# Optimization experiments

Hardware: AMD Instinct MI355X
Metric: run time of the kernel (lower is better)

Reference implementation:

```python
import jax, jax.numpy as jnp
import numpy as np
from jax import lax

B, C, H, W = 8, 256, 64, 64
NUM_HEADS = 4
HEAD_DIM = C // NUM_HEADS  # == dim // 4, required by q_proj
EPS_LN = 1e-5
EPS_NORM = 1e-12


def _gelu(x):
    return jax.nn.gelu(x, approximate=False)  # torch default GELU is erf-based


def setup_inputs() -> dict:
    key = jax.random.key(0)
    ks = jax.random.split(key, 20)
    s = lambda fan_in: 1.0 / np.sqrt(fan_in)
    return {
        "x": jax.random.normal(ks[0], (B, C, H, W), jnp.float32),
        # LayerNorm(dim)
        "ln_g": jnp.ones((C,), jnp.float32),
        "ln_b": jnp.zeros((C,), jnp.float32),
        # qkv: Linear(C, 3C, bias=False); stored (in, out)
        "w_qkv": jax.random.normal(ks[1], (C, 3 * C), jnp.float32) * s(C),
        # q_proj: Linear(head_dim, head_dim); stored (in, out)
        "w_q": jax.random.normal(ks[2], (HEAD_DIM, HEAD_DIM), jnp.float32) * s(HEAD_DIM),
        "b_q": jax.random.normal(ks[3], (HEAD_DIM,), jnp.float32) * 0.01,
        "temperature": jnp.ones((NUM_HEADS, 1, 1), jnp.float32),
        # depthwise 3x3 conv, groups=C: kernel (C,1,3,3) OIHW
        "dw_w": jax.random.normal(ks[4], (C, 1, 3, 3), jnp.float32) * s(9),
        "dw_b": jax.random.normal(ks[5], (C,), jnp.float32) * 0.01,
        # channel_interaction: 1x1 convs stored as (out, in)
        "ci_w1": jax.random.normal(ks[6], (C // 8, C), jnp.float32) * s(C),
        "ci_b1": jax.random.normal(ks[7], (C // 8,), jnp.float32) * 0.01,
        "ci_w2": jax.random.normal(ks[8], (C, C // 8), jnp.float32) * s(C // 8),
        "ci_b2": jax.random.normal(ks[9], (C,), jnp.float32) * 0.01,
        # spatial_interaction: 1x1 convs stored as (out, in)
        "si_w1": jax.random.normal(ks[10], (C // 16, C), jnp.float32) * s(C),
        "si_b1": jax.random.normal(ks[11], (C // 16,), jnp.float32) * 0.01,
        "si_w2": jax.random.normal(ks[12], (1, C // 16), jnp.float32) * s(C // 16),
        "si_b2": jax.random.normal(ks[13], (1,), jnp.float32) * 0.01,
        # proj: Linear(C, C); stored (in, out)
        "proj_w": jax.random.normal(ks[14], (C, C), jnp.float32) * s(C),
        "proj_b": jax.random.normal(ks[15], (C,), jnp.float32) * 0.01,
    }


def reference(x, ln_g, ln_b, w_qkv, w_q, b_q, temperature, dw_w, dw_b,
              ci_w1, ci_b1, ci_w2, ci_b2, si_w1, si_b1, si_w2, si_b2,
              proj_w, proj_b):
    Bx, Cx, Hx, Wx = x.shape
    N = Hx * Wx
    nh = temperature.shape[0]
    hd = Cx // nh

    # before_RG: (B,C,H,W) -> (B,N,C), LayerNorm over C
    xt = x.reshape(Bx, Cx, N).transpose(0, 2, 1)
    mu = xt.mean(-1, keepdims=True)
    var = ((xt - mu) ** 2).mean(-1, keepdims=True)
    xn = (xt - mu) * lax.rsqrt(var + EPS_LN) * ln_g + ln_b

    # qkv -> (3, B, nh, N, hd)
    qkv = (xn @ w_qkv).reshape(Bx, N, 3, nh, hd).transpose(2, 0, 3, 1, 4)
    q, k, v = qkv[0], qkv[1], qkv[2]
    q = q @ w_q + b_q                      # Linear on head_dim
    q = q.transpose(0, 1, 3, 2)            # (B, nh, hd, N)
    k = k.transpose(0, 1, 3, 2)
    v = v.transpose(0, 1, 3, 2)
    v_ = v.reshape(Bx, Cx, Hx, Wx)         # head-major channel layout

    # L2 normalize along N (torch F.normalize semantics)
    q = q / jnp.clip(jnp.linalg.norm(q, axis=-1, keepdims=True), EPS_NORM)
    k = k / jnp.clip(jnp.linalg.norm(k, axis=-1, keepdims=True), EPS_NORM)

    # channel attention: (B, nh, hd, hd)
    attn = jnp.einsum('bhdn,bhen->bhde', q, k) * temperature
    attn = jax.nn.softmax(attn, axis=-1)
    attened_x = jnp.einsum('bhde,bhen->bhdn', attn, v)
    attened_x = attened_x.transpose(0, 3, 1, 2).reshape(Bx, N, Cx)  # (B,N,C)

    # depthwise conv branch + GELU
    conv_x = lax.conv_general_dilated(
        v_, dw_w, window_strides=(1, 1), padding='SAME',
        feature_group_count=Cx, dimension_numbers=('NCHW', 'OIHW', 'NCHW'))
    conv_x = _gelu(conv_x + dw_b[None, :, None, None])

    # channel interaction (SE on attention branch)
    pooled = attened_x.mean(axis=1)                    # (B,C) == global avg pool of (B,C,H,W)
    ci = _gelu(pooled @ ci_w1.T + ci_b1)
    channel_map = ci @ ci_w2.T + ci_b2                 # (B,C)

    # spatial interaction (on conv branch)
    si = _gelu(jnp.einsum('bchw,oc->bohw', conv_x, si_w1) + si_b1[None, :, None, None])
    spatial_map = jnp.einsum('bchw,oc->bohw', si, si_w2) + si_b2[None, :, None, None]  # (B,1,H,W)
    spatial_map = spatial_map.reshape(Bx, N, 1)

    # cross gating and fuse
    attened_x = attened_x * jax.nn.sigmoid(spatial_map)
    conv_x = conv_x * jax.nn.sigmoid(channel_map)[:, :, None, None]
    conv_x = conv_x.reshape(Bx, Cx, N).transpose(0, 2, 1)

    out = (attened_x + conv_x) @ proj_w + proj_b       # (B,N,C)
    return out.transpose(0, 2, 1).reshape(Bx, Cx, Hx, Wx)
```

## Files before the change

### kernel.cpp

```cpp
#include <hip/hip_runtime.h>

typedef unsigned short u16;
typedef short bf16x8 __attribute__((ext_vector_type(8)));
typedef float f32x4 __attribute__((ext_vector_type(4)));

__device__ __forceinline__ float bf2f(u16 u){ return __uint_as_float(((unsigned)u)<<16); }
__device__ __forceinline__ u16 f2bf(float f){
  unsigned u = __float_as_uint(f);
  u += 0x7FFF + ((u >> 16) & 1);
  return (u16)(u >> 16);
}
__device__ __forceinline__ float ldp(const void* p, size_t i, int bf){
  return bf ? bf2f(((const u16*)p)[i]) : ((const float*)p)[i];
}
__device__ __forceinline__ float gelu_f(float x){ return 0.5f*x*(1.0f+erff(x*0.70710678118654752440f)); }
__device__ __forceinline__ float sigmoid_f(float x){ return 1.0f/(1.0f+expf(-x)); }

struct __align__(8)  U16x4 { u16 x,y,z,w; };
struct __align__(16) U16x8 { u16 v[8]; };

#define Cc 256
#define Nn 4096
#define CN 1048576


__global__ void k_flag(const unsigned* __restrict__ g_bits, int* __restrict__ flag){
  if (threadIdx.x == 0)
    *flag = (g_bits[0] == 0x3F803F80u) ? 1 : 0;
}

__global__ void k_zero(float* __restrict__ p){
  size_t i = ((size_t)blockIdx.x*256 + threadIdx.x)*4;
  float4 z; z.x=0.f; z.y=0.f; z.z=0.f; z.w=0.f;
  *(float4*)(p + i) = z;
}

__global__ void k_prep(const void* __restrict__ wqkv, const void* __restrict__ wq,
                       const void* __restrict__ bq, const void* __restrict__ pw,
                       const int* __restrict__ flag,
                       u16* __restrict__ WallT16, u16* __restrict__ pwT16,
                       float* __restrict__ biasall){
  int bf = *flag;
  int j = blockIdx.x;
  int c = threadIdx.x;
  if (j < 768){
    float out;
    if (j < 256){
      int h = j >> 6, e = j & 63;
      float acc = 0.f;
      #pragma unroll 8
      for (int d = 0; d < 64; ++d)
        acc += ldp(wqkv, c*768 + h*64 + d, bf) * ldp(wq, d*64 + e, bf);
      out = acc;
    } else {
      out = ldp(wqkv, c*768 + j, bf);
    }
    size_t a = ((size_t)((j>>4)*8 + (c>>5))*64 + (j&15) + 16*((c>>3)&3))*8 + (c&7);
    WallT16[a] = f2bf(out);
    if (c == 0) biasall[j] = (j < 256) ? ldp(bq, j & 63, bf) : 0.f;
  } else {
    int o = j - 768;
    size_t a = ((size_t)((o>>4)*8 + (c>>5))*64 + (o&15) + 16*((c>>3)&3))*8 + (c&7);
    pwT16[a] = f2bf(ldp(pw, c*256 + o, bf));
  }
}

__global__ __launch_bounds__(256) void k_lnT(const void* __restrict__ x,
                    const void* __restrict__ g, const void* __restrict__ bta,
                    const int* __restrict__ flag,
                    u16* __restrict__ xn16){
  __shared__ float tile[256*65];
  __shared__ float gs[256], bs[256];
  __shared__ float red_s[4][64], red_ss[4][64];
  __shared__ float mu_sh[64], rs_sh[64];
  int bf = *flag;
  int tid = threadIdx.x;
  int b  = blockIdx.x >> 6;
  int n0 = (blockIdx.x & 63) * 64;
  gs[tid] = ldp(g, tid, bf); bs[tid] = ldp(bta, tid, bf);
  int crow = tid >> 2, noff = (tid & 3) * 16;
  for (int p = 0; p < 4; ++p){
    int c = p*64 + crow;
    size_t base = (size_t)b*CN + (size_t)c*Nn + n0 + noff;
    float vals[16];
    if (bf){
      #pragma unroll
      for (int q = 0; q < 2; ++q){
        U16x8 u = *(const U16x8*)((const u16*)x + base + q*8);
        #pragma unroll
        for (int i = 0; i < 8; ++i) vals[q*8+i] = bf2f(u.v[i]);
      }
    } else {
      #pragma unroll
      for (int q = 0; q < 4; ++q){
        float4 f = *(const float4*)((const float*)x + base + q*4);
        vals[q*4+0]=f.x; vals[q*4+1]=f.y; vals[q*4+2]=f.z; vals[q*4+3]=f.w;
      }
    }
    #pragma unroll
    for (int i = 0; i < 16; ++i) tile[c*65 + noff + i] = vals[i];
  }
  __syncthreads();
  {
    int r = tid >> 6, nl = tid & 63;
    float s = 0.f, ss = 0.f;
    for (int cc = r*64; cc < r*64 + 64; ++cc){
      float v = tile[cc*65 + nl];
      s += v; ss += v*v;
    }
    red_s[r][nl] = s; red_ss[r][nl] = ss;
  }
  __syncthreads();
  if (tid < 64){
    float st  = red_s[0][tid]  + red_s[1][tid]  + red_s[2][tid]  + red_s[3][tid];
    float sst = red_ss[0][tid] + red_ss[1][tid] + red_ss[2][tid] + red_ss[3][tid];
    float m   = st * (1.f/256.f);
    float var = sst * (1.f/256.f) - m*m;
    mu_sh[tid] = m;
    rs_sh[tid] = rsqrtf(var + 1e-5f);
  }
  __syncthreads();
  int n = tid >> 2, coff = (tid & 3) * 64;
  float mn = mu_sh[n], rn = rs_sh[n];
  int gidx = (n0 >> 4) + (n >> 4);
  int l15 = n & 15;
  u16* dstb = xn16 + ((size_t)b*256 + gidx)*4096;
  for (int q = 0; q < 8; ++q){
    int c8 = coff + q*8;
    int ks = c8 >> 5, quad = (c8 >> 3) & 3;
    U16x8 w;
    #pragma unroll
    for (int i = 0; i < 8; ++i){
      int c = c8 + i;
      w.v[i] = f2bf((tile[c*65 + n] - mn)*rn*gs[c] + bs[c]);
    }
    *(U16x8*)(dstb + (size_t)ks*512 + (l15 + 16*quad)*8) = w;
  }
}

__global__ __launch_bounds__(256, 4) void k_qkv(const u16* __restrict__ xn16,
                                             const u16* __restrict__ WallT16,
                                             const float* __restrict__ biasall,
                                             u16* __restrict__ q16, u16* __restrict__ k16,
                                             u16* __restrict__ v16, u16* __restrict__ vT16,
                                             float* __restrict__ qsq, float* __restrict__ ksq){
  __shared__ u16 Bs[16384];
  __shared__ float bias_sh[64];
  __shared__ float sq_sh[64];
  int tid = threadIdx.x;
  int by = blockIdx.x;
  int bx = blockIdx.y;
  int b  = by >> 5;
  int n0 = (by & 31) * 128;
  int j0 = bx * 64;
  int part = bx >> 2;
  int h = (j0 >> 6) & 3;
  int w = tid >> 6, lane = tid & 63, l15 = lane & 15, quad = lane >> 4;

  const u16* Afrag = xn16 + ((size_t)b*256 + (n0>>4) + w*2)*4096 + lane*8;
  bf16x8 af[2][8];
  #pragma unroll
  for (int r = 0; r < 2; ++r)
    #pragma unroll
    for (int ks = 0; ks < 8; ++ks)
      af[r][ks] = *(const bf16x8*)(Afrag + (size_t)r*4096 + (size_t)ks*512);

  const u16* Bt = WallT16 + (size_t)(j0>>4)*4096;
  #pragma unroll
  for (int i = 0; i < 8; ++i){
    int off = (i*256 + tid)*8;
    *(bf16x8*)(Bs + off) = *(const bf16x8*)(Bt + off);
  }
  if (tid < 64){ bias_sh[tid] = biasall[j0 + tid]; sq_sh[tid] = 0.f; }
  __syncthreads();

  f32x4 acc[2][4];
  #pragma unroll
  for (int r=0;r<2;++r)
    #pragma unroll
    for (int s=0;s<4;++s){ acc[r][s][0]=0.f; acc[r][s][1]=0.f; acc[r][s][2]=0.f; acc[r][s][3]=0.f; }

  const u16* Bfrag = Bs + lane*8;
  #pragma unroll
  for (int ks = 0; ks < 8; ++ks){
    #pragma unroll
    for (int s = 0; s < 4; ++s){
      bf16x8 bb = *(const bf16x8*)(Bfrag + s*4096 + ks*512);
      acc[0][s] = __builtin_amdgcn_mfma_f32_16x16x32_bf16(af[0][ks], bb, acc[0][s], 0, 0, 0);
      acc[1][s] = __builtin_amdgcn_mfma_f32_16x16x32_bf16(af[1][ks], bb, acc[1][s], 0, 0, 0);
    }
  }
  u16* dst = (part==0) ? q16 : ((part==1) ? k16 : v16);
  float sql[4];
  #pragma unroll
  for (int s=0;s<4;++s) sql[s]=0.f;
  #pragma unroll
  for (int r = 0; r < 2; ++r){
    int nb = n0 + w*32 + r*16 + quad*4;
    #pragma unroll
    for (int s = 0; s < 4; ++s){
      int d = s*16 + l15;
      float bd = bias_sh[d];
      float v0 = acc[r][s][0] + bd, v1 = acc[r][s][1] + bd;
      float v2 = acc[r][s][2] + bd, v3 = acc[r][s][3] + bd;
      U16x4 wv; wv.x=f2bf(v0); wv.y=f2bf(v1); wv.z=f2bf(v2); wv.w=f2bf(v3);
      *(U16x4*)(dst + ((size_t)(b*4 + h)*64 + d)*4096 + nb) = wv;
      sql[s] += v0*v0 + v1*v1 + v2*v2 + v3*v3;
    }
  }
  if (part < 2){
    #pragma unroll
    for (int s = 0; s < 4; ++s)
      atomicAdd(&sq_sh[s*16 + l15], sql[s]);
    __syncthreads();
    if (tid < 64){
      float* nsq = (part==0) ? qsq : ksq;
      atomicAdd(&nsq[(b*4 + h)*64 + tid], sq_sh[tid]);
    }
  } else {
    __syncthreads();
    u16* Ls = Bs;
    #pragma unroll
    for (int r = 0; r < 2; ++r){
      #pragma unroll
      for (int s = 0; s < 4; ++s){
        int d = s*16 + l15;
        #pragma unroll
        for (int i = 0; i < 4; ++i){
          int nl = w*32 + r*16 + quad*4 + i;
          Ls[nl*72 + d] = f2bf(acc[r][s][i]);
        }
      }
    }
    __syncthreads();
    u16* vt = vT16 + ((size_t)(b*4 + h))*262144 + (size_t)(n0>>4)*1024;
    #pragma unroll
    for (int it = 0; it < 4; ++it){
      int lin = it*256 + tid;
      int t15 = lin & 15, q4 = (lin>>4)&3, ks = (lin>>6)&1, g = lin>>7;
      int nl = g*16 + t15;
      int e0 = ks*32 + q4*8;
      U16x8 wv = *(const U16x8*)&Ls[nl*72 + e0];
      *(U16x8*)(vt + (size_t)lin*8) = wv;
    }
  }
}

__global__ __launch_bounds__(256) void k_attnp(const u16* __restrict__ q16,
                                               const u16* __restrict__ k16,
                                               float* __restrict__ S){
  int tid = threadIdx.x;
  int bh = blockIdx.y;
  int kc = blockIdx.x;
  int w = tid >> 6, lane = tid & 63, l15 = lane & 15, quad = lane >> 4;
  f32x4 acc[4];
  #pragma unroll
  for (int s=0;s<4;++s){ acc[s][0]=0.f; acc[s][1]=0.f; acc[s][2]=0.f; acc[s][3]=0.f; }
  const u16* qp = q16 + ((size_t)bh*64 + w*16 + l15)*4096 + quad*8;
  const u16* kp = k16 + ((size_t)bh*64 + l15)*4096 + quad*8;
  #pragma unroll 4
  for (int nn = kc*512; nn < kc*512 + 512; nn += 32){
    bf16x8 a = *(const bf16x8*)(qp + nn);
    #pragma unroll
    for (int s = 0; s < 4; ++s){
      bf16x8 bb = *(const bf16x8*)(kp + (size_t)s*16*4096 + nn);
      acc[s] = __builtin_amdgcn_mfma_f32_16x16x32_bf16(a, bb, acc[s], 0, 0, 0);
    }
  }
  float* Sb = S + (size_t)bh*4096;
  #pragma unroll
  for (int s = 0; s < 4; ++s)
    #pragma unroll
    for (int i = 0; i < 4; ++i)
      atomicAdd(&Sb[(w*16 + quad*4 + i)*64 + s*16 + l15], acc[s][i]);
}

__global__ __launch_bounds__(256) void k_softmax(float* __restrict__ S,
                          const float* __restrict__ qsq, const float* __restrict__ ksq,
                          const void* __restrict__ temp, const int* __restrict__ flag,
                          u16* __restrict__ P16){
  __shared__ float kn_sh[64], qn_sh[64];
  int bf = *flag;
  int bh = blockIdx.x;
  int tid = threadIdx.x;
  if (tid < 64){
    kn_sh[tid] = fmaxf(sqrtf(ksq[bh*64 + tid]), 1e-12f);
    qn_sh[tid] = fmaxf(sqrtf(qsq[bh*64 + tid]), 1e-12f);
  }
  __syncthreads();
  int d  = tid >> 2;
  int e0 = (tid & 3) * 16;
  float tpr = ldp(temp, bh & 3, bf);
  const float* row = S + (size_t)bh*4096 + d*64 + e0;
  float sc = tpr / qn_sh[d];
  float v[16];
  #pragma unroll
  for (int q = 0; q < 4; ++q){
    float4 f = *(const float4*)(row + q*4);
    v[q*4+0]=f.x; v[q*4+1]=f.y; v[q*4+2]=f.z; v[q*4+3]=f.w;
  }
  float mx = -1e30f;
  #pragma unroll
  for (int e = 0; e < 16; ++e){
    v[e] = v[e] * sc / kn_sh[e0 + e];
    mx = fmaxf(mx, v[e]);
  }
  mx = fmaxf(mx, __shfl_xor(mx, 1));
  mx = fmaxf(mx, __shfl_xor(mx, 2));
  float s = 0.f;
  #pragma unroll
  for (int e = 0; e < 16; ++e){ v[e] = expf(v[e] - mx); s += v[e]; }
  s += __shfl_xor(s, 1);
  s += __shfl_xor(s, 2);
  float inv = 1.f/s;
  u16* pb16 = P16 + bh*4096;
  int g = d >> 4, l15d = d & 15;
  #pragma unroll
  for (int half = 0; half < 2; ++half){
    int e = e0 + half*8;
    int ks = e >> 5, q4 = (e >> 3) & 3;
    U16x8 wv;
    #pragma unroll
    for (int i = 0; i < 8; ++i) wv.v[i] = f2bf(v[half*8 + i]*inv);
    *(U16x8*)(pb16 + ((g*2 + ks)*64 + l15d + 16*q4)*8) = wv;
  }
}

__global__ __launch_bounds__(256) void k_av(const u16* __restrict__ P16,
                                            const u16* __restrict__ vT16,
                                            u16* __restrict__ attT,
                                            float* __restrict__ pooled){
  __shared__ u16 Bs[16384];
  __shared__ float red[64];
  int bh = blockIdx.y;
  int n0 = blockIdx.x * 256;
  int tid = threadIdx.x, w = tid >> 6, lane = tid & 63, l15 = lane & 15, quad = lane >> 4;
  int b = bh >> 2, h = bh & 3;
  const u16* vt = vT16 + (size_t)bh*262144 + (size_t)(n0>>4)*1024;
  #pragma unroll
  for (int i = 0; i < 8; ++i){
    int off = (i*256 + tid)*8;
    *(bf16x8*)(Bs + off) = *(const bf16x8*)(vt + off);
  }
  if (tid < 64) red[tid] = 0.f;
  const u16* pp = P16 + bh*4096;
  bf16x8 af0 = *(const bf16x8*)(pp + ((w*2 + 0)*64 + lane)*8);
  bf16x8 af1 = *(const bf16x8*)(pp + ((w*2 + 1)*64 + lane)*8);
  __syncthreads();
  f32x4 acc[16];
  #pragma unroll
  for (int s = 0; s < 16; ++s){ acc[s][0]=0.f; acc[s][1]=0.f; acc[s][2]=0.f; acc[s][3]=0.f; }
  const u16* Bfrag = Bs + lane*8;
  #pragma unroll
  for (int s = 0; s < 16; ++s){
    bf16x8 b0 = *(const bf16x8*)(Bfrag + (s*2 + 0)*512);
    bf16x8 b1 = *(const bf16x8*)(Bfrag + (s*2 + 1)*512);
    acc[s] = __builtin_amdgcn_mfma_f32_16x16x32_bf16(af0, b0, acc[s], 0, 0, 0);
    acc[s] = __builtin_amdgcn_mfma_f32_16x16x32_bf16(af1, b1, acc[s], 0, 0, 0);
  }
  u16* ob = attT + ((size_t)b*4096 + n0)*256 + h*64 + w*16 + quad*4;
  float p0=0.f, p1=0.f, p2=0.f, p3=0.f;
  #pragma unroll
  for (int s = 0; s < 16; ++s){
    int n = s*16 + l15;
    U16x4 wv; wv.x=f2bf(acc[s][0]); wv.y=f2bf(acc[s][1]); wv.z=f2bf(acc[s][2]); wv.w=f2bf(acc[s][3]);
    *(U16x4*)(ob + (size_t)n*256) = wv;
    p0 += acc[s][0]; p1 += acc[s][1]; p2 += acc[s][2]; p3 += acc[s][3];
  }
  atomicAdd(&red[w*16 + quad*4 + 0], p0);
  atomicAdd(&red[w*16 + quad*4 + 1], p1);
  atomicAdd(&red[w*16 + quad*4 + 2], p2);
  atomicAdd(&red[w*16 + quad*4 + 3], p3);
  __syncthreads();
  if (tid < 64)
    atomicAdd(&pooled[b*256 + h*64 + tid], red[tid]);
}

__global__ void k_conv(const u16* __restrict__ v16, const void* __restrict__ dww,
                       const void* __restrict__ dwb, const int* __restrict__ flag,
                       u16* __restrict__ conv16){
  __shared__ float plane[4096];
  int bf = *flag;
  int bc = blockIdx.x;
  int c = bc & 255;
  int tid = threadIdx.x;
  const u16* vp = v16 + (size_t)bc*4096;
  #pragma unroll
  for (int i = 0; i < 4; ++i){
    int lin = (i*256 + tid)*4;
    U16x4 vu = *(const U16x4*)(vp + lin);
    plane[lin+0]=bf2f(vu.x); plane[lin+1]=bf2f(vu.y); plane[lin+2]=bf2f(vu.z); plane[lin+3]=bf2f(vu.w);
  }
  float wgt[9];
  #pragma unroll
  for (int i = 0; i < 9; ++i) wgt[i] = ldp(dww, c*9 + i, bf);
  float bias = ldp(dwb, c, bf);
  __syncthreads();
  u16* op = conv16 + (size_t)bc*4096;
  for (int it = 0; it < 16; ++it){
    int p = it*256 + tid;
    int y = p >> 6, x = p & 63;
    float acc = bias;
    #pragma unroll
    for (int ky = 0; ky < 3; ++ky){
      int yy = y + ky - 1;
      if (yy < 0 || yy > 63) continue;
      #pragma unroll
      for (int kx = 0; kx < 3; ++kx){
        int xx = x + kx - 1;
        if (xx < 0 || xx > 63) continue;
        acc += wgt[ky*3+kx]*plane[yy*64 + xx];
      }
    }
    op[p] = f2bf(gelu_f(acc));
  }
}

__global__ __launch_bounds__(256) void k_spatial(const u16* __restrict__ conv16,
                                                 const void* __restrict__ w1, const void* __restrict__ b1,
                                                 const void* __restrict__ w2, const void* __restrict__ b2,
                                                 const int* __restrict__ flag,
                                                 float* __restrict__ ssp){
  __shared__ float w1s[16][256];
  __shared__ u16 tile[256][72];
  __shared__ float red[4][64][17];
  int bf = *flag;
  int tid = threadIdx.x;
  for (int i = 0; i < 16; ++i)
    w1s[i][tid] = ldp(w1, i*256 + tid, bf);
  int b  = blockIdx.x >> 6;
  int n0 = (blockIdx.x & 63) * 64;
  const u16* cb = conv16 + (size_t)b*CN + n0;
  #pragma unroll
  for (int i = 0; i < 8; ++i){
    int idx = i*256 + tid;
    int c = idx >> 3, seg = idx & 7;
    *(U16x8*)&tile[c][seg*8] = *(const U16x8*)(cb + (size_t)c*Nn + seg*8);
  }
  __syncthreads();
  int nl = tid & 63, r = tid >> 6;
  float acc[16] = {};
  for (int cc = r*64; cc < r*64 + 64; ++cc){
    float xv = bf2f(tile[cc][nl]);
    #pragma unroll
    for (int o = 0; o < 16; ++o) acc[o] += xv * w1s[o][cc];
  }
  #pragma unroll
  for (int o = 0; o < 16; ++o) red[r][nl][o] = acc[o];
  __syncthreads();
  if (tid < 64){
    float sp = ldp(b2, 0, bf);
    #pragma unroll
    for (int o = 0; o < 16; ++o){
      float a = red[0][tid][o] + red[1][tid][o] + red[2][tid][o] + red[3][tid][o];
      sp += gelu_f(a + ldp(b1, o, bf)) * ldp(w2, o, bf);
    }
    ssp[(size_t)b*Nn + n0 + tid] = sigmoid_f(sp);
  }
}

__global__ void k_channel(const float* __restrict__ pooled,
                          const void* __restrict__ w1, const void* __restrict__ b1,
                          const void* __restrict__ w2, const void* __restrict__ b2,
                          const int* __restrict__ flag,
                          float* __restrict__ sch){
  __shared__ float ps[256];
  __shared__ float cis[32];
  int bf = *flag;
  int b = blockIdx.x, tid = threadIdx.x;
  ps[tid] = pooled[b*256 + tid] * (1.f/4096.f);
  __syncthreads();
  if (tid < 32){
    float a = ldp(b1, tid, bf);
    for (int cc = 0; cc < 256; ++cc) a += ps[cc]*ldp(w1, tid*256 + cc, bf);
    cis[tid] = gelu_f(a);
  }
  __syncthreads();
  float m = ldp(b2, tid, bf);
  #pragma unroll
  for (int o = 0; o < 32; ++o) m += cis[o]*ldp(w2, tid*32 + o, bf);
  sch[b*256 + tid] = sigmoid_f(m);
}

__global__ __launch_bounds__(256) void k_gate(const u16* __restrict__ attT,
                                              const u16* __restrict__ conv16,
                                              const float* __restrict__ ssp,
                                              const float* __restrict__ sch,
                                              u16* __restrict__ Y16){
  __shared__ u16 ct[256*66];
  __shared__ u16 at[64*264];
  __shared__ float ssp_sh[64], sch_sh[256];
  int tid = threadIdx.x;
  int b  = blockIdx.x >> 6;
  int n0 = (blockIdx.x & 63) * 64;
  sch_sh[tid] = sch[b*256 + tid];
  if (tid < 64) ssp_sh[tid] = ssp[(size_t)b*Nn + n0 + tid];
  const u16* cb = conv16 + (size_t)b*CN + n0;
  #pragma unroll
  for (int i = 0; i < 8; ++i){
    int idx = i*256 + tid;
    int c = idx >> 3, seg = idx & 7;
    *(U16x8*)&ct[c*66 + seg*8] = *(const U16x8*)(cb + (size_t)c*Nn + seg*8);
  }
  const u16* ab = attT + ((size_t)b*4096 + n0)*256;
  #pragma unroll
  for (int i = 0; i < 8; ++i){
    int idx = i*256 + tid;
    int n = idx >> 5, seg = idx & 31;
    *(U16x8*)&at[n*264 + seg*8] = *(const U16x8*)(ab + (size_t)n*256 + seg*8);
  }
  __syncthreads();
  u16* dstb = Y16 + ((size_t)b*256 + (n0>>4))*4096;
  #pragma unroll
  for (int it = 0; it < 8; ++it){
    int lin = it*256 + tid;
    int l15 = lin & 15, q4 = (lin>>4)&3, ks = (lin>>6)&7, ng = lin>>9;
    int n = ng*16 + l15;
    int c0 = ks*32 + q4*8;
    float gn = ssp_sh[n];
    U16x8 av = *(const U16x8*)&at[n*264 + c0];
    U16x8 wv;
    #pragma unroll
    for (int i = 0; i < 8; ++i){
      int c = c0 + i;
      wv.v[i] = f2bf(bf2f(av.v[i])*gn + bf2f(ct[c*66 + n])*sch_sh[c]);
    }
    *(U16x8*)(dstb + (size_t)lin*8) = wv;
  }
}

__global__ __launch_bounds__(256, 4) void k_proj(const u16* __restrict__ Y16,
                                              const u16* __restrict__ pwT16,
                                              const void* __restrict__ pb,
                                              const int* __restrict__ flag,
                                              void* __restrict__ out){
  __shared__ u16 Bs[16384];
  __shared__ float pb_sh[64];
  int bf = *flag;
  int tid = threadIdx.x;
  int by = blockIdx.x;
  int bx = blockIdx.y;
  int b  = by >> 5;
  int n0 = (by & 31) * 128;
  int c0 = bx * 64;
  int w = tid >> 6, lane = tid & 63, l15 = lane & 15, quad = lane >> 4;

  const u16* Afrag = Y16 + ((size_t)b*256 + (n0>>4) + w*2)*4096 + lane*8;
  bf16x8 af[2][8];
  #pragma unroll
  for (int r = 0; r < 2; ++r)
    #pragma unroll
    for (int ks = 0; ks < 8; ++ks)
      af[r][ks] = *(const bf16x8*)(Afrag + (size_t)r*4096 + (size_t)ks*512);

  const u16* Bt = pwT16 + (size_t)(c0>>4)*4096;
  #pragma unroll
  for (int i = 0; i < 8; ++i){
    int off = (i*256 + tid)*8;
    *(bf16x8*)(Bs + off) = *(const bf16x8*)(Bt + off);
  }
  if (tid < 64) pb_sh[tid] = ldp(pb, c0 + tid, bf);
  __syncthreads();

  f32x4 acc[2][4];
  #pragma unroll
  for (int r=0;r<2;++r)
    #pragma unroll
    for (int s=0;s<4;++s){ acc[r][s][0]=0.f; acc[r][s][1]=0.f; acc[r][s][2]=0.f; acc[r][s][3]=0.f; }

  const u16* Bfrag = Bs + lane*8;
  #pragma unroll
  for (int ks = 0; ks < 8; ++ks){
    #pragma unroll
    for (int s = 0; s < 4; ++s){
      bf16x8 bb = *(const bf16x8*)(Bfrag + s*4096 + ks*512);
      acc[0][s] = __builtin_amdgcn_mfma_f32_16x16x32_bf16(af[0][ks], bb, acc[0][s], 0, 0, 0);
      acc[1][s] = __builtin_amdgcn_mfma_f32_16x16x32_bf16(af[1][ks], bb, acc[1][s], 0, 0, 0);
    }
  }
  #pragma unroll
  for (int r = 0; r < 2; ++r){
    int nb = n0 + w*32 + r*16 + quad*4;
    #pragma unroll
    for (int s = 0; s < 4; ++s){
      int cch = c0 + s*16 + l15;
      float pbias = pb_sh[s*16 + l15];
      size_t oidx = ((size_t)(b*256 + cch))*4096 + nb;
      float v0 = acc[r][s][0] + pbias, v1 = acc[r][s][1] + pbias;
      float v2 = acc[r][s][2] + pbias, v3 = acc[r][s][3] + pbias;
      if (bf){
        U16x4 wv; wv.x=f2bf(v0); wv.y=f2bf(v1); wv.z=f2bf(v2); wv.w=f2bf(v3);
        *(U16x4*)((u16*)out + oidx) = wv;
      } else {
        float4 wv; wv.x=v0; wv.y=v1; wv.z=v2; wv.w=v3;
        *(float4*)((float*)out + oidx) = wv;
      }
    }
  }
}

extern "C" void kernel_launch(void* const* d_in, const int* in_sizes, int n_in,
                              void* d_out, int out_size, void* d_ws, size_t ws_size,
                              hipStream_t stream) {
  const void* x    = d_in[0];
  const void* ln_g = d_in[1];
  const void* ln_b = d_in[2];
  const void* wqkv = d_in[3];
  const void* wq   = d_in[4];
  const void* bq   = d_in[5];
  const void* temp = d_in[6];
  const void* dww  = d_in[7];
  const void* dwb  = d_in[8];
  const void* ciw1 = d_in[9];
  const void* cib1 = d_in[10];
  const void* ciw2 = d_in[11];
  const void* cib2 = d_in[12];
  const void* siw1 = d_in[13];
  const void* sib1 = d_in[14];
  const void* siw2 = d_in[15];
  const void* sib2 = d_in[16];
  const void* pw   = d_in[17];
  const void* pb   = d_in[18];

  u16* wsu    = (u16*)d_ws;
  u16* q16    = wsu;
  u16* k16    = wsu + 8388608;
  u16* xn16   = wsu + 16777216;
  u16* attT   = q16;
  u16* conv16 = k16;
  u16* Y16    = xn16;
  u16* v16    = (u16*)d_out;

  u16* vT16;
  if (out_size >= 33554432) vT16 = (u16*)d_out + 8388608;
  else                      vT16 = wsu + 25165824;

  float* tail = (float*)(wsu + 33554432);
  float* qsq  = tail;
  float* ksq  = qsq + 2048;
  float* S    = ksq + 2048;
  float* pool = S + 131072;
  float* biasall = pool + 2048;
  float* sch  = biasall + 768;
  float* ssp  = sch + 2048;
  u16* P16     = (u16*)(ssp + 32768);
  u16* WallT16 = P16 + 131072;
  u16* pwT16   = WallT16 + 196608;
  int* flag    = (int*)(pwT16 + 65536);

  hipLaunchKernelGGL(k_flag,  dim3(1), dim3(64), 0, stream, (const unsigned*)ln_g, flag);
  hipLaunchKernelGGL(k_zero,  dim3(134), dim3(256), 0, stream, qsq);
  hipLaunchKernelGGL(k_prep,  dim3(1024), dim3(256), 0, stream, wqkv, wq, bq, pw, flag, WallT16, pwT16, biasall);
  hipLaunchKernelGGL(k_lnT,   dim3(512), dim3(256), 0, stream, x, ln_g, ln_b, flag, xn16);
  hipLaunchKernelGGL(k_qkv,   dim3(256, 12), dim3(256), 0, stream,
                     xn16, WallT16, biasall, q16, k16, v16, vT16, qsq, ksq);
  hipLaunchKernelGGL(k_attnp, dim3(8, 32), dim3(256), 0, stream, q16, k16, S);
  hipLaunchKernelGGL(k_softmax, dim3(32), dim3(256), 0, stream, S, qsq, ksq, temp, flag, P16);
  hipLaunchKernelGGL(k_av,    dim3(16, 32), dim3(256), 0, stream, P16, vT16, attT, pool);
  hipLaunchKernelGGL(k_conv,  dim3(2048), dim3(256), 0, stream, v16, dww, dwb, flag, conv16);
  hipLaunchKernelGGL(k_spatial, dim3(512), dim3(256), 0, stream, conv16, siw1, sib1, siw2, sib2, flag, ssp);
  hipLaunchKernelGGL(k_channel, dim3(8), dim3(256), 0, stream, pool, ciw1, cib1, ciw2, cib2, flag, sch);
  hipLaunchKernelGGL(k_gate,  dim3(512), dim3(256), 0, stream, attT, conv16, ssp, sch, Y16);
  hipLaunchKernelGGL(k_proj,  dim3(256, 4), dim3(256), 0, stream, Y16, pwT16, pb, flag, d_out);
}
```

Measured before the change: 291.4 us.

## Fuse attention stages, gate+projection, and inline dtype flag; vectorize depthwise conv

Merges the three attention kernels (partial QK^T with global atomics, softmax, AV) into one per-(batch,head) kernel that keeps scores and probabilities in shared memory. It also fuses the gating kernel into the output projection, keeping the gated tile in LDS. The flag and zero kernels are removed: the dtype test is done inline and zeroing moves into the prep kernel. The depthwise conv now computes 16 outputs per thread from register rows. The fused attention kernel runs only 32 blocks, so GPU occupancy drops sharply in exchange for fewer launches and fewer global round trips.

```diff
diff --git a/kernel.cpp b/kernel.cpp
--- a/kernel.cpp
+++ b/kernel.cpp
@@ -15,6 +15,7 @@
 }
 __device__ __forceinline__ float gelu_f(float x){ return 0.5f*x*(1.0f+erff(x*0.70710678118654752440f)); }
 __device__ __forceinline__ float sigmoid_f(float x){ return 1.0f/(1.0f+expf(-x)); }
+__device__ __forceinline__ int bfdet(const void* g){ return ((const unsigned*)g)[0] == 0x3F803F80u; }
 
 struct __align__(8)  U16x4 { u16 x,y,z,w; };
 struct __align__(16) U16x8 { u16 v[8]; };
@@ -24,25 +25,20 @@
 #define CN 1048576
 
 
-__global__ void k_flag(const unsigned* __restrict__ g_bits, int* __restrict__ flag){
-  if (threadIdx.x == 0)
-    *flag = (g_bits[0] == 0x3F803F80u) ? 1 : 0;
-}
-
-__global__ void k_zero(float* __restrict__ p){
-  size_t i = ((size_t)blockIdx.x*256 + threadIdx.x)*4;
-  float4 z; z.x=0.f; z.y=0.f; z.z=0.f; z.w=0.f;
-  *(float4*)(p + i) = z;
-}
-
 __global__ void k_prep(const void* __restrict__ wqkv, const void* __restrict__ wq,
                        const void* __restrict__ bq, const void* __restrict__ pw,
-                       const int* __restrict__ flag,
+                       const unsigned* __restrict__ g_bits,
                        u16* __restrict__ WallT16, u16* __restrict__ pwT16,
-                       float* __restrict__ biasall){
-  int bf = *flag;
+                       float* __restrict__ biasall, float* __restrict__ zbase){
   int j = blockIdx.x;
   int c = threadIdx.x;
+  if (j >= 1024){
+    size_t i = (size_t)(j - 1024)*1024 + c*4;
+    float4 z; z.x=0.f; z.y=0.f; z.z=0.f; z.w=0.f;
+    *(float4*)(zbase + i) = z;
+    return;
+  }
+  int bf = bfdet(g_bits);
   if (j < 768){
     float out;
     if (j < 256){
@@ -67,13 +63,12 @@
 
 __global__ __launch_bounds__(256) void k_lnT(const void* __restrict__ x,
                     const void* __restrict__ g, const void* __restrict__ bta,
-                    const int* __restrict__ flag,
                     u16* __restrict__ xn16){
   __shared__ float tile[256*65];
   __shared__ float gs[256], bs[256];
   __shared__ float red_s[4][64], red_ss[4][64];
   __shared__ float mu_sh[64], rs_sh[64];
-  int bf = *flag;
+  int bf = bfdet(g);
   int tid = threadIdx.x;
   int b  = blockIdx.x >> 6;
   int n0 = (blockIdx.x & 63) * 64;
@@ -246,20 +241,38 @@
   }
 }
 
-__global__ __launch_bounds__(256) void k_attnp(const u16* __restrict__ q16,
-                                               const u16* __restrict__ k16,
-                                               float* __restrict__ S){
+__global__ __launch_bounds__(512) void k_attn(const u16* __restrict__ q16,
+                                              const u16* __restrict__ k16,
+                                              const u16* __restrict__ vT16,
+                                              const float* __restrict__ qsq,
+                                              const float* __restrict__ ksq,
+                                              const void* __restrict__ temp,
+                                              const unsigned* __restrict__ g_bits,
+                                              u16* __restrict__ attT,
+                                              float* __restrict__ pooled){
+  __shared__ float S_sh[2][64][68];
+  __shared__ u16 P_sh[4096];
+  __shared__ float kn_sh[64], qn_sh[64];
+  __shared__ float red[64];
+  int bf = bfdet(g_bits);
+  int bh = blockIdx.x; int b = bh >> 2, h = bh & 3;
   int tid = threadIdx.x;
-  int bh = blockIdx.y;
-  int kc = blockIdx.x;
-  int w = tid >> 6, lane = tid & 63, l15 = lane & 15, quad = lane >> 4;
+  int w2 = tid >> 6, lane = tid & 63, l15 = lane & 15, quad = lane >> 4;
+  int dg = w2 & 3, nh = w2 >> 2;
+
+  if (tid < 64){
+    kn_sh[tid] = fmaxf(sqrtf(ksq[bh*64 + tid]), 1e-12f);
+    qn_sh[tid] = fmaxf(sqrtf(qsq[bh*64 + tid]), 1e-12f);
+    red[tid] = 0.f;
+  }
+
   f32x4 acc[4];
   #pragma unroll
   for (int s=0;s<4;++s){ acc[s][0]=0.f; acc[s][1]=0.f; acc[s][2]=0.f; acc[s][3]=0.f; }
-  const u16* qp = q16 + ((size_t)bh*64 + w*16 + l15)*4096 + quad*8;
-  const u16* kp = k16 + ((size_t)bh*64 + l15)*4096 + quad*8;
+  const u16* qp = q16 + ((size_t)bh*64 + dg*16 + l15)*4096 + quad*8 + nh*2048;
+  const u16* kp = k16 + ((size_t)bh*64 + l15)*4096 + quad*8 + nh*2048;
   #pragma unroll 4
-  for (int nn = kc*512; nn < kc*512 + 512; nn += 32){
+  for (int nn = 0; nn < 2048; nn += 32){
     bf16x8 a = *(const bf16x8*)(qp + nn);
     #pragma unroll
     for (int s = 0; s < 4; ++s){
@@ -267,120 +280,87 @@
       acc[s] = __builtin_amdgcn_mfma_f32_16x16x32_bf16(a, bb, acc[s], 0, 0, 0);
     }
   }
-  float* Sb = S + (size_t)bh*4096;
   #pragma unroll
   for (int s = 0; s < 4; ++s)
     #pragma unroll
     for (int i = 0; i < 4; ++i)
-      atomicAdd(&Sb[(w*16 + quad*4 + i)*64 + s*16 + l15], acc[s][i]);
-}
-
-__global__ __launch_bounds__(256) void k_softmax(float* __restrict__ S,
-                          const float* __restrict__ qsq, const float* __restrict__ ksq,
-                          const void* __restrict__ temp, const int* __restrict__ flag,
-                          u16* __restrict__ P16){
-  __shared__ float kn_sh[64], qn_sh[64];
-  int bf = *flag;
-  int bh = blockIdx.x;
-  int tid = threadIdx.x;
-  if (tid < 64){
-    kn_sh[tid] = fmaxf(sqrtf(ksq[bh*64 + tid]), 1e-12f);
-    qn_sh[tid] = fmaxf(sqrtf(qsq[bh*64 + tid]), 1e-12f);
-  }
-  __syncthreads();
-  int d  = tid >> 2;
-  int e0 = (tid & 3) * 16;
-  float tpr = ldp(temp, bh & 3, bf);
-  const float* row = S + (size_t)bh*4096 + d*64 + e0;
-  float sc = tpr / qn_sh[d];
-  float v[16];
-  #pragma unroll
-  for (int q = 0; q < 4; ++q){
-    float4 f = *(const float4*)(row + q*4);
-    v[q*4+0]=f.x; v[q*4+1]=f.y; v[q*4+2]=f.z; v[q*4+3]=f.w;
-  }
-  float mx = -1e30f;
-  #pragma unroll
-  for (int e = 0; e < 16; ++e){
-    v[e] = v[e] * sc / kn_sh[e0 + e];
-    mx = fmaxf(mx, v[e]);
-  }
-  mx = fmaxf(mx, __shfl_xor(mx, 1));
-  mx = fmaxf(mx, __shfl_xor(mx, 2));
-  float s = 0.f;
-  #pragma unroll
-  for (int e = 0; e < 16; ++e){ v[e] = expf(v[e] - mx); s += v[e]; }
-  s += __shfl_xor(s, 1);
-  s += __shfl_xor(s, 2);
-  float inv = 1.f/s;
-  u16* pb16 = P16 + bh*4096;
-  int g = d >> 4, l15d = d & 15;
-  #pragma unroll
-  for (int half = 0; half < 2; ++half){
-    int e = e0 + half*8;
-    int ks = e >> 5, q4 = (e >> 3) & 3;
+      S_sh[nh][dg*16 + quad*4 + i][s*16 + l15] = acc[s][i];
+  __syncthreads();
+
+  {
+    int d = tid >> 3, el = tid & 7, e0 = el*8;
+    float tpr = ldp(temp, h, bf);
+    float sc = tpr / qn_sh[d];
+    float v[8];
+    float4 a0 = *(const float4*)&S_sh[0][d][e0];
+    float4 a1 = *(const float4*)&S_sh[0][d][e0+4];
+    float4 b0 = *(const float4*)&S_sh[1][d][e0];
+    float4 b1 = *(const float4*)&S_sh[1][d][e0+4];
+    v[0]=a0.x+b0.x; v[1]=a0.y+b0.y; v[2]=a0.z+b0.z; v[3]=a0.w+b0.w;
+    v[4]=a1.x+b1.x; v[5]=a1.y+b1.y; v[6]=a1.z+b1.z; v[7]=a1.w+b1.w;
+    float mx = -1e30f;
+    #pragma unroll
+    for (int e = 0; e < 8; ++e){
+      v[e] = v[e] * sc / kn_sh[e0 + e];
+      mx = fmaxf(mx, v[e]);
+    }
+    mx = fmaxf(mx, __shfl_xor(mx, 1));
+    mx = fmaxf(mx, __shfl_xor(mx, 2));
+    mx = fmaxf(mx, __shfl_xor(mx, 4));
+    float s = 0.f;
+    #pragma unroll
+    for (int e = 0; e < 8; ++e){ v[e] = expf(v[e] - mx); s += v[e]; }
+    s += __shfl_xor(s, 1);
+    s += __shfl_xor(s, 2);
+    s += __shfl_xor(s, 4);
+    float inv = 1.f/s;
+    int g = d >> 4, l15d = d & 15, ks = el >> 2, q4 = el & 3;
     U16x8 wv;
     #pragma unroll
-    for (int i = 0; i < 8; ++i) wv.v[i] = f2bf(v[half*8 + i]*inv);
-    *(U16x8*)(pb16 + ((g*2 + ks)*64 + l15d + 16*q4)*8) = wv;
-  }
-}
-
-__global__ __launch_bounds__(256) void k_av(const u16* __restrict__ P16,
-                                            const u16* __restrict__ vT16,
-                                            u16* __restrict__ attT,
-                                            float* __restrict__ pooled){
-  __shared__ u16 Bs[16384];
-  __shared__ float red[64];
-  int bh = blockIdx.y;
-  int n0 = blockIdx.x * 256;
-  int tid = threadIdx.x, w = tid >> 6, lane = tid & 63, l15 = lane & 15, quad = lane >> 4;
-  int b = bh >> 2, h = bh & 3;
-  const u16* vt = vT16 + (size_t)bh*262144 + (size_t)(n0>>4)*1024;
-  #pragma unroll
-  for (int i = 0; i < 8; ++i){
-    int off = (i*256 + tid)*8;
-    *(bf16x8*)(Bs + off) = *(const bf16x8*)(vt + off);
-  }
-  if (tid < 64) red[tid] = 0.f;
-  const u16* pp = P16 + bh*4096;
-  bf16x8 af0 = *(const bf16x8*)(pp + ((w*2 + 0)*64 + lane)*8);
-  bf16x8 af1 = *(const bf16x8*)(pp + ((w*2 + 1)*64 + lane)*8);
-  __syncthreads();
-  f32x4 acc[16];
-  #pragma unroll
-  for (int s = 0; s < 16; ++s){ acc[s][0]=0.f; acc[s][1]=0.f; acc[s][2]=0.f; acc[s][3]=0.f; }
-  const u16* Bfrag = Bs + lane*8;
-  #pragma unroll
-  for (int s = 0; s < 16; ++s){
-    bf16x8 b0 = *(const bf16x8*)(Bfrag + (s*2 + 0)*512);
-    bf16x8 b1 = *(const bf16x8*)(Bfrag + (s*2 + 1)*512);
-    acc[s] = __builtin_amdgcn_mfma_f32_16x16x32_bf16(af0, b0, acc[s], 0, 0, 0);
-    acc[s] = __builtin_amdgcn_mfma_f32_16x16x32_bf16(af1, b1, acc[s], 0, 0, 0);
-  }
-  u16* ob = attT + ((size_t)b*4096 + n0)*256 + h*64 + w*16 + quad*4;
-  float p0=0.f, p1=0.f, p2=0.f, p3=0.f;
-  #pragma unroll
-  for (int s = 0; s < 16; ++s){
-    int n = s*16 + l15;
-    U16x4 wv; wv.x=f2bf(acc[s][0]); wv.y=f2bf(acc[s][1]); wv.z=f2bf(acc[s][2]); wv.w=f2bf(acc[s][3]);
-    *(U16x4*)(ob + (size_t)n*256) = wv;
-    p0 += acc[s][0]; p1 += acc[s][1]; p2 += acc[s][2]; p3 += acc[s][3];
-  }
-  atomicAdd(&red[w*16 + quad*4 + 0], p0);
-  atomicAdd(&red[w*16 + quad*4 + 1], p1);
-  atomicAdd(&red[w*16 + quad*4 + 2], p2);
-  atomicAdd(&red[w*16 + quad*4 + 3], p3);
+    for (int i = 0; i < 8; ++i) wv.v[i] = f2bf(v[i]*inv);
+    *(U16x8*)(P_sh + ((g*2 + ks)*64 + l15d + 16*q4)*8) = wv;
+  }
+  __syncthreads();
+
+  bf16x8 af[4][2];
+  #pragma unroll
+  for (int mg = 0; mg < 4; ++mg)
+    #pragma unroll
+    for (int ks = 0; ks < 2; ++ks)
+      af[mg][ks] = *(const bf16x8*)(P_sh + ((mg*2 + ks)*64 + lane)*8);
+  const u16* vt = vT16 + (size_t)bh*262144;
+  float ps[4][4] = {};
+  for (int g64 = 0; g64 < 32; ++g64){
+    int gidx = w2*32 + g64;
+    bf16x8 b0 = *(const bf16x8*)(vt + (size_t)gidx*1024 + lane*8);
+    bf16x8 b1 = *(const bf16x8*)(vt + (size_t)gidx*1024 + 512 + lane*8);
+    int n = gidx*16 + l15;
+    u16* ob = attT + ((size_t)b*4096 + n)*256 + h*64 + quad*4;
+    #pragma unroll
+    for (int mg = 0; mg < 4; ++mg){
+      f32x4 o; o[0]=0.f; o[1]=0.f; o[2]=0.f; o[3]=0.f;
+      o = __builtin_amdgcn_mfma_f32_16x16x32_bf16(af[mg][0], b0, o, 0, 0, 0);
+      o = __builtin_amdgcn_mfma_f32_16x16x32_bf16(af[mg][1], b1, o, 0, 0, 0);
+      U16x4 wv; wv.x=f2bf(o[0]); wv.y=f2bf(o[1]); wv.z=f2bf(o[2]); wv.w=f2bf(o[3]);
+      *(U16x4*)(ob + mg*16) = wv;
+      ps[mg][0] += o[0]; ps[mg][1] += o[1]; ps[mg][2] += o[2]; ps[mg][3] += o[3];
+    }
+  }
+  #pragma unroll
+  for (int mg = 0; mg < 4; ++mg)
+    #pragma unroll
+    for (int i = 0; i < 4; ++i)
+      atomicAdd(&red[mg*16 + quad*4 + i], ps[mg][i]);
   __syncthreads();
   if (tid < 64)
     atomicAdd(&pooled[b*256 + h*64 + tid], red[tid]);
 }
 
-__global__ void k_conv(const u16* __restrict__ v16, const void* __restrict__ dww,
-                       const void* __restrict__ dwb, const int* __restrict__ flag,
+__global__ __launch_bounds__(256) void k_conv(const u16* __restrict__ v16, const void* __restrict__ dww,
+                       const void* __restrict__ dwb, const unsigned* __restrict__ g_bits,
                        u16* __restrict__ conv16){
   __shared__ float plane[4096];
-  int bf = *flag;
+  int bf = bfdet(g_bits);
   int bc = blockIdx.x;
   int c = bc & 255;
   int tid = threadIdx.x;
@@ -396,35 +376,51 @@
   for (int i = 0; i < 9; ++i) wgt[i] = ldp(dww, c*9 + i, bf);
   float bias = ldp(dwb, c, bf);
   __syncthreads();
-  u16* op = conv16 + (size_t)bc*4096;
-  for (int it = 0; it < 16; ++it){
-    int p = it*256 + tid;
-    int y = p >> 6, x = p & 63;
+  int y = tid >> 2, x0 = (tid & 3) * 16;
+  float r[3][18];
+  #pragma unroll
+  for (int ky = 0; ky < 3; ++ky){
+    int yy = y + ky - 1;
+    if (yy < 0 || yy > 63){
+      #pragma unroll
+      for (int j = 0; j < 18; ++j) r[ky][j] = 0.f;
+    } else {
+      const float* rp = &plane[yy*64 + x0];
+      r[ky][0]  = (x0 == 0)  ? 0.f : rp[-1];
+      r[ky][17] = (x0 == 48) ? 0.f : rp[16];
+      #pragma unroll
+      for (int q = 0; q < 4; ++q){
+        float4 f = *(const float4*)(rp + q*4);
+        r[ky][1+q*4+0]=f.x; r[ky][1+q*4+1]=f.y; r[ky][1+q*4+2]=f.z; r[ky][1+q*4+3]=f.w;
+      }
+    }
+  }
+  U16x8 o0, o1;
+  #pragma unroll
+  for (int x = 0; x < 16; ++x){
     float acc = bias;
     #pragma unroll
-    for (int ky = 0; ky < 3; ++ky){
-      int yy = y + ky - 1;
-      if (yy < 0 || yy > 63) continue;
+    for (int ky = 0; ky < 3; ++ky)
       #pragma unroll
-      for (int kx = 0; kx < 3; ++kx){
-        int xx = x + kx - 1;
-        if (xx < 0 || xx > 63) continue;
-        acc += wgt[ky*3+kx]*plane[yy*64 + xx];
-      }
-    }
-    op[p] = f2bf(gelu_f(acc));
-  }
+      for (int kx = 0; kx < 3; ++kx)
+        acc += wgt[ky*3+kx] * r[ky][x+kx];
+    u16 ov = f2bf(gelu_f(acc));
+    if (x < 8) o0.v[x] = ov; else o1.v[x-8] = ov;
+  }
+  u16* op = conv16 + (size_t)bc*4096 + y*64 + x0;
+  *(U16x8*)op = o0;
+  *(U16x8*)(op + 8) = o1;
 }
 
 __global__ __launch_bounds__(256) void k_spatial(const u16* __restrict__ conv16,
                                                  const void* __restrict__ w1, const void* __restrict__ b1,
                                                  const void* __restrict__ w2, const void* __restrict__ b2,
-                                                 const int* __restrict__ flag,
+                                                 const unsigned* __restrict__ g_bits,
                                                  float* __restrict__ ssp){
   __shared__ float w1s[16][256];
   __shared__ u16 tile[256][72];
   __shared__ float red[4][64][17];
-  int bf = *flag;
+  int bf = bfdet(g_bits);
   int tid = threadIdx.x;
   for (int i = 0; i < 16; ++i)
     w1s[i][tid] = ldp(w1, i*256 + tid, bf);
@@ -462,11 +458,11 @@
 __global__ void k_channel(const float* __restrict__ pooled,
                           const void* __restrict__ w1, const void* __restrict__ b1,
                           const void* __restrict__ w2, const void* __restrict__ b2,
-                          const int* __restrict__ flag,
+                          const unsigned* __restrict__ g_bits,
                           float* __restrict__ sch){
   __shared__ float ps[256];
   __shared__ float cis[32];
-  int bf = *flag;
+  int bf = bfdet(g_bits);
   int b = blockIdx.x, tid = threadIdx.x;
   ps[tid] = pooled[b*256 + tid] * (1.f/4096.f);
   __syncthreads();
@@ -482,40 +478,47 @@
   sch[b*256 + tid] = sigmoid_f(m);
 }
 
-__global__ __launch_bounds__(256) void k_gate(const u16* __restrict__ attT,
-                                              const u16* __restrict__ conv16,
-                                              const float* __restrict__ ssp,
-                                              const float* __restrict__ sch,
-                                              u16* __restrict__ Y16){
-  __shared__ u16 ct[256*66];
+__global__ __launch_bounds__(512) void k_out(const u16* __restrict__ attT,
+                                             const u16* __restrict__ conv16,
+                                             const float* __restrict__ ssp,
+                                             const float* __restrict__ sch,
+                                             const u16* __restrict__ pwT16,
+                                             const void* __restrict__ pb,
+                                             const unsigned* __restrict__ g_bits,
+                                             void* __restrict__ out){
+  __shared__ u16 ct[256*72];
   __shared__ u16 at[64*264];
-  __shared__ float ssp_sh[64], sch_sh[256];
+  __shared__ u16 Yf[32768];
+  __shared__ float ssp_sh[64], sch_sh[256], pb_sh[256];
+  int bf = bfdet(g_bits);
   int tid = threadIdx.x;
   int b  = blockIdx.x >> 6;
   int n0 = (blockIdx.x & 63) * 64;
-  sch_sh[tid] = sch[b*256 + tid];
+  int w2 = tid >> 6, lane = tid & 63, l15 = lane & 15, quad = lane >> 4;
+  int mg = w2 & 3, chalf = w2 >> 2;
+
+  if (tid < 256){ sch_sh[tid] = sch[b*256 + tid]; pb_sh[tid] = ldp(pb, tid, bf); }
   if (tid < 64) ssp_sh[tid] = ssp[(size_t)b*Nn + n0 + tid];
   const u16* cb = conv16 + (size_t)b*CN + n0;
   #pragma unroll
-  for (int i = 0; i < 8; ++i){
-    int idx = i*256 + tid;
+  for (int i = 0; i < 4; ++i){
+    int idx = i*512 + tid;
     int c = idx >> 3, seg = idx & 7;
-    *(U16x8*)&ct[c*66 + seg*8] = *(const U16x8*)(cb + (size_t)c*Nn + seg*8);
+    *(U16x8*)&ct[c*72 + seg*8] = *(const U16x8*)(cb + (size_t)c*Nn + seg*8);
   }
   const u16* ab = attT + ((size_t)b*4096 + n0)*256;
   #pragma unroll
-  for (int i = 0; i < 8; ++i){
-    int idx = i*256 + tid;
+  for (int i = 0; i < 4; ++i){
+    int idx = i*512 + tid;
     int n = idx >> 5, seg = idx & 31;
     *(U16x8*)&at[n*264 + seg*8] = *(const U16x8*)(ab + (size_t)n*256 + seg*8);
   }
   __syncthreads();
-  u16* dstb = Y16 + ((size_t)b*256 + (n0>>4))*4096;
-  #pragma unroll
-  for (int it = 0; it < 8; ++it){
-    int lin = it*256 + tid;
-    int l15 = lin & 15, q4 = (lin>>4)&3, ks = (lin>>6)&7, ng = lin>>9;
-    int n = ng*16 + l15;
+  #pragma unroll
+  for (int it = 0; it < 4; ++it){
+    int lin = it*512 + tid;
+    int tl15 = lin & 15, q4 = (lin>>4)&3, ks = (lin>>6)&7, ng = lin>>9;
+    int n = ng*16 + tl15;
     int c0 = ks*32 + q4*8;
     float gn = ssp_sh[n];
     U16x8 av = *(const U16x8*)&at[n*264 + c0];
@@ -523,78 +526,41 @@
     #pragma unroll
     for (int i = 0; i < 8; ++i){
       int c = c0 + i;
-      wv.v[i] = f2bf(bf2f(av.v[i])*gn + bf2f(ct[c*66 + n])*sch_sh[c]);
-    }
-    *(U16x8*)(dstb + (size_t)lin*8) = wv;
-  }
-}
-
-__global__ __launch_bounds__(256, 4) void k_proj(const u16* __restrict__ Y16,
-                                              const u16* __restrict__ pwT16,
-                                              const void* __restrict__ pb,
-                                              const int* __restrict__ flag,
-                                              void* __restrict__ out){
-  __shared__ u16 Bs[16384];
-  __shared__ float pb_sh[64];
-  int bf = *flag;
-  int tid = threadIdx.x;
-  int by = blockIdx.x;
-  int bx = blockIdx.y;
-  int b  = by >> 5;
-  int n0 = (by & 31) * 128;
-  int c0 = bx * 64;
-  int w = tid >> 6, lane = tid & 63, l15 = lane & 15, quad = lane >> 4;
-
-  const u16* Afrag = Y16 + ((size_t)b*256 + (n0>>4) + w*2)*4096 + lane*8;
-  bf16x8 af[2][8];
-  #pragma unroll
-  for (int r = 0; r < 2; ++r)
-    #pragma unroll
-    for (int ks = 0; ks < 8; ++ks)
-      af[r][ks] = *(const bf16x8*)(Afrag + (size_t)r*4096 + (size_t)ks*512);
-
-  const u16* Bt = pwT16 + (size_t)(c0>>4)*4096;
-  #pragma unroll
-  for (int i = 0; i < 8; ++i){
-    int off = (i*256 + tid)*8;
-    *(bf16x8*)(Bs + off) = *(const bf16x8*)(Bt + off);
-  }
-  if (tid < 64) pb_sh[tid] = ldp(pb, c0 + tid, bf);
-  __syncthreads();
-
-  f32x4 acc[2][4];
-  #pragma unroll
-  for (int r=0;r<2;++r)
-    #pragma unroll
-    for (int s=0;s<4;++s){ acc[r][s][0]=0.f; acc[r][s][1]=0.f; acc[r][s][2]=0.f; acc[r][s][3]=0.f; }
-
-  const u16* Bfrag = Bs + lane*8;
-  #pragma unroll
-  for (int ks = 0; ks < 8; ++ks){
-    #pragma unroll
-    for (int s = 0; s < 4; ++s){
-      bf16x8 bb = *(const bf16x8*)(Bfrag + s*4096 + ks*512);
-      acc[0][s] = __builtin_amdgcn_mfma_f32_16x16x32_bf16(af[0][ks], bb, acc[0][s], 0, 0, 0);
-      acc[1][s] = __builtin_amdgcn_mfma_f32_16x16x32_bf16(af[1][ks], bb, acc[1][s], 0, 0, 0);
-    }
-  }
-  #pragma unroll
-  for (int r = 0; r < 2; ++r){
-    int nb = n0 + w*32 + r*16 + quad*4;
-    #pragma unroll
-    for (int s = 0; s < 4; ++s){
-      int cch = c0 + s*16 + l15;
-      float pbias = pb_sh[s*16 + l15];
-      size_t oidx = ((size_t)(b*256 + cch))*4096 + nb;
-      float v0 = acc[r][s][0] + pbias, v1 = acc[r][s][1] + pbias;
-      float v2 = acc[r][s][2] + pbias, v3 = acc[r][s][3] + pbias;
-      if (bf){
-        U16x4 wv; wv.x=f2bf(v0); wv.y=f2bf(v1); wv.z=f2bf(v2); wv.w=f2bf(v3);
-        *(U16x4*)((u16*)out + oidx) = wv;
-      } else {
-        float4 wv; wv.x=v0; wv.y=v1; wv.z=v2; wv.w=v3;
-        *(float4*)((float*)out + oidx) = wv;
-      }
+      wv.v[i] = f2bf(bf2f(av.v[i])*gn + bf2f(ct[c*72 + n])*sch_sh[c]);
+    }
+    *(U16x8*)(Yf + (size_t)lin*8) = wv;
+  }
+  __syncthreads();
+  bf16x8 af[8];
+  #pragma unroll
+  for (int ks = 0; ks < 8; ++ks)
+    af[ks] = *(const bf16x8*)(Yf + ((size_t)(mg*8 + ks)*64 + lane)*8);
+  f32x4 acc[8];
+  #pragma unroll
+  for (int s=0;s<8;++s){ acc[s][0]=0.f; acc[s][1]=0.f; acc[s][2]=0.f; acc[s][3]=0.f; }
+  #pragma unroll
+  for (int sl = 0; sl < 8; ++sl){
+    int s = chalf*8 + sl;
+    #pragma unroll
+    for (int ks = 0; ks < 8; ++ks){
+      bf16x8 bb = *(const bf16x8*)(pwT16 + ((size_t)(s*8 + ks))*512 + lane*8);
+      acc[sl] = __builtin_amdgcn_mfma_f32_16x16x32_bf16(af[ks], bb, acc[sl], 0, 0, 0);
+    }
+  }
+  int nbase = n0 + mg*16 + quad*4;
+  #pragma unroll
+  for (int sl = 0; sl < 8; ++sl){
+    int cout = chalf*128 + sl*16 + l15;
+    float pbias = pb_sh[cout];
+    size_t oidx = ((size_t)(b*256 + cout))*4096 + nbase;
+    float v0 = acc[sl][0] + pbias, v1 = acc[sl][1] + pbias;
+    float v2 = acc[sl][2] + pbias, v3 = acc[sl][3] + pbias;
+    if (bf){
+      U16x4 wv; wv.x=f2bf(v0); wv.y=f2bf(v1); wv.z=f2bf(v2); wv.w=f2bf(v3);
+      *(U16x4*)((u16*)out + oidx) = wv;
+    } else {
+      float4 wv; wv.x=v0; wv.y=v1; wv.z=v2; wv.w=v3;
+      *(float4*)((float*)out + oidx) = wv;
     }
   }
 }
@@ -628,7 +594,6 @@
   u16* xn16   = wsu + 16777216;
   u16* attT   = q16;
   u16* conv16 = k16;
-  u16* Y16    = xn16;
   u16* v16    = (u16*)d_out;
 
   u16* vT16;
@@ -638,28 +603,26 @@
   float* tail = (float*)(wsu + 33554432);
   float* qsq  = tail;
   float* ksq  = qsq + 2048;
-  float* S    = ksq + 2048;
-  float* pool = S + 131072;
+  float* pool = ksq + 2048;
   float* biasall = pool + 2048;
   float* sch  = biasall + 768;
   float* ssp  = sch + 2048;
-  u16* P16     = (u16*)(ssp + 32768);
-  u16* WallT16 = P16 + 131072;
+  u16* WallT16 = (u16*)(ssp + 32768);
   u16* pwT16   = WallT16 + 196608;
-  int* flag    = (int*)(pwT16 + 65536);
-
-  hipLaunchKernelGGL(k_flag,  dim3(1), dim3(64), 0, stream, (const unsigned*)ln_g, flag);
-  hipLaunchKernelGGL(k_zero,  dim3(134), dim3(256), 0, stream, qsq);
-  hipLaunchKernelGGL(k_prep,  dim3(1024), dim3(256), 0, stream, wqkv, wq, bq, pw, flag, WallT16, pwT16, biasall);
-  hipLaunchKernelGGL(k_lnT,   dim3(512), dim3(256), 0, stream, x, ln_g, ln_b, flag, xn16);
+
+  hipLaunchKernelGGL(k_prep,  dim3(1030), dim3(256), 0, stream, wqkv, wq, bq, pw,
+                     (const unsigned*)ln_g, WallT16, pwT16, biasall, qsq);
+  hipLaunchKernelGGL(k_lnT,   dim3(512), dim3(256), 0, stream, x, ln_g, ln_b, xn16);
   hipLaunchKernelGGL(k_qkv,   dim3(256, 12), dim3(256), 0, stream,
                      xn16, WallT16, biasall, q16, k16, v16, vT16, qsq, ksq);
-  hipLaunchKernelGGL(k_attnp, dim3(8, 32), dim3(256), 0, stream, q16, k16, S);
-  hipLaunchKernelGGL(k_softmax, dim3(32), dim3(256), 0, stream, S, qsq, ksq, temp, flag, P16);
-  hipLaunchKernelGGL(k_av,    dim3(16, 32), dim3(256), 0, stream, P16, vT16, attT, pool);
-  hipLaunchKernelGGL(k_conv,  dim3(2048), dim3(256), 0, stream, v16, dww, dwb, flag, conv16);
-  hipLaunchKernelGGL(k_spatial, dim3(512), dim3(256), 0, stream, conv16, siw1, sib1, siw2, sib2, flag, ssp);
-  hipLaunchKernelGGL(k_channel, dim3(8), dim3(256), 0, stream, pool, ciw1, cib1, ciw2, cib2, flag, sch);
-  hipLaunchKernelGGL(k_gate,  dim3(512), dim3(256), 0, stream, attT, conv16, ssp, sch, Y16);
-  hipLaunchKernelGGL(k_proj,  dim3(256, 4), dim3(256), 0, stream, Y16, pwT16, pb, flag, d_out);
-}
+  hipLaunchKernelGGL(k_attn,  dim3(32), dim3(512), 0, stream,
+                     q16, k16, vT16, qsq, ksq, temp, (const unsigned*)ln_g, attT, pool);
+  hipLaunchKernelGGL(k_conv,  dim3(2048), dim3(256), 0, stream, v16, dww, dwb,
+                     (const unsigned*)ln_g, conv16);
+  hipLaunchKernelGGL(k_spatial, dim3(512), dim3(256), 0, stream, conv16, siw1, sib1, siw2, sib2,
+                     (const unsigned*)ln_g, ssp);
+  hipLaunchKernelGGL(k_channel, dim3(8), dim3(256), 0, stream, pool, ciw1, cib1, ciw2, cib2,
+                     (const unsigned*)ln_g, sch);
+  hipLaunchKernelGGL(k_out,   dim3(512), dim3(512), 0, stream, attT, conv16, ssp, sch,
+                     pwT16, pb, (const unsigned*)ln_g, d_out);
+}
```

Result: slower. 387.8 us (+33.1%).
